# Performance work log

Measured on AMD Instinct MI355X. Metric: run time of the kernel, lower is better.

The kernel has to match this reference:

```python
import jax, jax.numpy as jnp
import numpy as np


def setup_inputs() -> dict:
    key = jax.random.key(0)
    k1, k2 = jax.random.split(key)
    B, N, C = 16, 2049, 1024
    x = jax.random.normal(k1, (B, N, C), dtype=jnp.float32)
    # nn.Linear(dim, 3*dim, bias=False): weight applied as x @ W^T; store as (C, 3C)
    w_qkv = jax.random.normal(k2, (C, 3 * C), dtype=jnp.float32) * (1.0 / np.sqrt(C))
    return {"x": x, "w_qkv": w_qkv}


def reference(x, w_qkv):
    B, N, C = x.shape
    scale = C ** (-0.5)
    qkv = (x @ w_qkv).reshape(B, N, 3, C)  # [B,N,3,C]
    q = qkv[:, :, 0, :]  # [B,N,C]
    k = qkv[:, :, 1, :]  # [B,N,C]
    # Original computes full q @ k^T then keeps only row 0, cols 1: before softmax.
    # Mathematically identical (and efficient) to use only the CLS query row.
    q_cls = q[:, 0, :]                                   # [B,C]
    attn_cls_logits = jnp.einsum('bc,bnc->bn', q_cls, k[:, 1:, :]) * scale  # [B,N-1]
    return jax.nn.softmax(attn_cls_logits, axis=-1)
```

## Files before the change

### kernel.cpp

```cpp
#include <hip/hip_runtime.h>
#include <math.h>


#define BATCH 16
#define SEQ   2049
#define CH    1024
#define W3    3072
#define NOUT  2048


__global__ __launch_bounds__(64) void qcls_partial_kernel(
    const float* __restrict__ x, const float* __restrict__ w,
    float* __restrict__ part) {
    const int ci = blockIdx.x;
    const int pi = blockIdx.y;
    const int lane = threadIdx.x;
    const int d0 = pi * 16;
    __shared__ float xs[BATCH * 16];
    #pragma unroll
    for (int i = lane; i < BATCH * 16; i += 64) {
        const int b = i >> 4, dd = i & 15;
        xs[i] = x[(size_t)b * SEQ * CH + d0 + dd];
    }
    __syncthreads();
    const int c = ci * 256 + lane * 4;
    float4 acc[BATCH];
    #pragma unroll
    for (int b = 0; b < BATCH; ++b) acc[b] = {0.f, 0.f, 0.f, 0.f};
    #pragma unroll 4
    for (int dd = 0; dd < 16; ++dd) {
        const float4 wv = *(const float4*)(w + (size_t)(d0 + dd) * W3 + c);
        #pragma unroll
        for (int b = 0; b < BATCH; ++b) {
            const float s = xs[b * 16 + dd];
            acc[b].x += s * wv.x; acc[b].y += s * wv.y;
            acc[b].z += s * wv.z; acc[b].w += s * wv.w;
        }
    }
    #pragma unroll
    for (int b = 0; b < BATCH; ++b)
        *(float4*)(part + (size_t)pi * BATCH * CH + b * CH + c) = acc[b];
}

__global__ __launch_bounds__(256) void qcls_reduce_kernel(
    const float* __restrict__ part, float* __restrict__ qcls) {
    const int id = blockIdx.x * 256 + threadIdx.x;
    float s = 0.f;
    #pragma unroll 8
    for (int p = 0; p < 64; ++p) s += part[(size_t)p * BATCH * CH + id];
    qcls[id] = s;
}

__global__ __launch_bounds__(256) void v_kernel(
    const float* __restrict__ w, const float* __restrict__ qcls,
    float* __restrict__ v) {
    __shared__ float qs[BATCH * CH];
    const int t = threadIdx.x;
    for (int i = t; i < BATCH * CH; i += 256) qs[i] = qcls[i];
    __syncthreads();
    const int lane = t & 63;
    const int wave = t >> 6;
    #pragma unroll
    for (int k = 0; k < 2; ++k) {
        const int d = blockIdx.x * 8 + wave * 2 + k;
        const float* wrow = w + (size_t)d * W3 + CH;
        float4 wv[4];
        #pragma unroll
        for (int j = 0; j < 4; ++j)
            wv[j] = *(const float4*)(wrow + lane * 4 + j * 256);
        #pragma unroll
        for (int b = 0; b < BATCH; ++b) {
            float acc = 0.f;
            #pragma unroll
            for (int j = 0; j < 4; ++j) {
                float4 qv = *(const float4*)(&qs[b * CH + lane * 4 + j * 256]);
                acc += wv[j].x * qv.x + wv[j].y * qv.y
                     + wv[j].z * qv.z + wv[j].w * qv.w;
            }
            #pragma unroll
            for (int off = 32; off > 0; off >>= 1)
                acc += __shfl_down(acc, off, 64);
            if (lane == 0) v[b * CH + d] = acc;
        }
    }
}

__global__ __launch_bounds__(256) void logits_kernel(
    const float* __restrict__ x, const float* __restrict__ v,
    float* __restrict__ logits) {
    const int t = threadIdx.x;
    const int lane = t & 63;
    const int row = blockIdx.x * 4 + (t >> 6);
    const int b = row >> 11;
    const int n = row & 2047;
    const float* xrow = x + ((size_t)b * SEQ + n + 1) * CH;
    const float* vrow = v + b * CH;
    float acc = 0.f;
    #pragma unroll
    for (int j = 0; j < 4; ++j) {
        float4 xv = *(const float4*)(xrow + lane * 4 + j * 256);
        float4 vv = *(const float4*)(vrow + lane * 4 + j * 256);
        acc += xv.x * vv.x + xv.y * vv.y + xv.z * vv.z + xv.w * vv.w;
    }
    #pragma unroll
    for (int off = 32; off > 0; off >>= 1)
        acc += __shfl_down(acc, off, 64);
    if (lane == 0) logits[row] = acc * 0.03125f;
}

__global__ __launch_bounds__(256) void softmax_kernel(
    const float* __restrict__ logits, float* __restrict__ out) {
    const int b = blockIdx.x;
    const int t = threadIdx.x;
    __shared__ float sm[256];
    float val[8];
    float m = -1e30f;
    #pragma unroll
    for (int i = 0; i < 8; ++i) {
        val[i] = logits[b * NOUT + t + i * 256];
        m = fmaxf(m, val[i]);
    }
    sm[t] = m; __syncthreads();
    for (int s = 128; s > 0; s >>= 1) {
        if (t < s) sm[t] = fmaxf(sm[t], sm[t + s]);
        __syncthreads();
    }
    const float mx = sm[0];
    __syncthreads();
    float e[8];
    float sum = 0.f;
    #pragma unroll
    for (int i = 0; i < 8; ++i) { e[i] = expf(val[i] - mx); sum += e[i]; }
    sm[t] = sum; __syncthreads();
    for (int s = 128; s > 0; s >>= 1) {
        if (t < s) sm[t] += sm[t + s];
        __syncthreads();
    }
    const float inv = 1.0f / sm[0];
    #pragma unroll
    for (int i = 0; i < 8; ++i) out[b * NOUT + t + i * 256] = e[i] * inv;
}

extern "C" void kernel_launch(void* const* d_in, const int* in_sizes, int n_in,
                              void* d_out, int out_size, void* d_ws, size_t ws_size,
                              hipStream_t stream) {
    const float* x = (const float*)d_in[0];
    const float* w = (const float*)d_in[1];
    float* out = (float*)d_out;
    float* ws = (float*)d_ws;

    float* part   = ws;
    float* qcls   = ws + 1048576;
    float* vbuf   = ws + 1048576 + 16384;
    float* logits = ws + 1048576 + 32768;

    qcls_partial_kernel<<<dim3(4, 64), 64, 0, stream>>>(x, w, part);
    qcls_reduce_kernel<<<64, 256, 0, stream>>>(part, qcls);
    v_kernel<<<128, 256, 0, stream>>>(w, qcls, vbuf);
    logits_kernel<<<8192, 256, 0, stream>>>(x, vbuf, logits);
    softmax_kernel<<<BATCH, 256, 0, stream>>>(logits, out);
}
```

Baseline: 219.4 us.

## Reduce q_cls partials in-block and fold final reduction into v kernel

The q_cls partial kernel now uses 512-thread blocks that split the D dimension across 8 waves and reduce across waves in shared memory, cutting partial slices from 64 to 8. The separate reduce kernel is dropped; v_kernel sums the 8 partials while loading q into shared memory and handles 16 rows per block over 64 blocks. logits_kernel stages the per-batch v vector in shared memory. The aim is to remove one launch and the partial-buffer traffic, at the cost of fewer blocks (32) in the first stage and 64 blocks redundantly reducing the partials.

```diff
diff --git a/kernel.cpp b/kernel.cpp
--- a/kernel.cpp
+++ b/kernel.cpp
@@ -7,75 +7,100 @@
 #define CH    1024
 #define W3    3072
 #define NOUT  2048
+#define PD    8
 
 
-__global__ __launch_bounds__(64) void qcls_partial_kernel(
+__global__ __launch_bounds__(512) void qcls_part_kernel(
     const float* __restrict__ x, const float* __restrict__ w,
     float* __restrict__ part) {
     const int ci = blockIdx.x;
     const int pi = blockIdx.y;
-    const int lane = threadIdx.x;
-    const int d0 = pi * 16;
-    __shared__ float xs[BATCH * 16];
-    #pragma unroll
-    for (int i = lane; i < BATCH * 16; i += 64) {
-        const int b = i >> 4, dd = i & 15;
-        xs[i] = x[(size_t)b * SEQ * CH + d0 + dd];
+    const int t  = threadIdx.x;
+    const int lane = t & 63;
+    const int wv   = t >> 6;
+
+    __shared__ float  xs[BATCH][128];
+    __shared__ float4 red[8][8][64];
+
+    for (int i = t; i < BATCH * 128; i += 512) {
+        const int b = i >> 7, dd = i & 127;
+        xs[b][dd] = x[(size_t)b * SEQ * CH + pi * 128 + dd];
     }
     __syncthreads();
+
     const int c = ci * 256 + lane * 4;
     float4 acc[BATCH];
     #pragma unroll
     for (int b = 0; b < BATCH; ++b) acc[b] = {0.f, 0.f, 0.f, 0.f};
+
+    const int drow0 = pi * 128 + wv * 16;
     #pragma unroll 4
     for (int dd = 0; dd < 16; ++dd) {
-        const float4 wv = *(const float4*)(w + (size_t)(d0 + dd) * W3 + c);
+        const float4 wvec = *(const float4*)(w + (size_t)(drow0 + dd) * W3 + c);
+        const int dl = wv * 16 + dd;
         #pragma unroll
         for (int b = 0; b < BATCH; ++b) {
-            const float s = xs[b * 16 + dd];
-            acc[b].x += s * wv.x; acc[b].y += s * wv.y;
-            acc[b].z += s * wv.z; acc[b].w += s * wv.w;
+            const float s = xs[b][dl];
+            acc[b].x += s * wvec.x; acc[b].y += s * wvec.y;
+            acc[b].z += s * wvec.z; acc[b].w += s * wvec.w;
         }
     }
+
     #pragma unroll
-    for (int b = 0; b < BATCH; ++b)
-        *(float4*)(part + (size_t)pi * BATCH * CH + b * CH + c) = acc[b];
-}
-
-__global__ __launch_bounds__(256) void qcls_reduce_kernel(
-    const float* __restrict__ part, float* __restrict__ qcls) {
-    const int id = blockIdx.x * 256 + threadIdx.x;
-    float s = 0.f;
-    #pragma unroll 8
-    for (int p = 0; p < 64; ++p) s += part[(size_t)p * BATCH * CH + id];
-    qcls[id] = s;
+    for (int p = 0; p < 2; ++p) {
+        #pragma unroll
+        for (int b2 = 0; b2 < 8; ++b2)
+            red[wv][b2][lane] = acc[p * 8 + b2];
+        __syncthreads();
+        {
+            const int b = p * 8 + wv;
+            float4 s = red[0][wv][lane];
+            #pragma unroll
+            for (int ww = 1; ww < 8; ++ww) {
+                const float4 r = red[ww][wv][lane];
+                s.x += r.x; s.y += r.y; s.z += r.z; s.w += r.w;
+            }
+            *(float4*)(part + ((size_t)pi * BATCH + b) * CH + c) = s;
+        }
+        __syncthreads();
+    }
 }
 
 __global__ __launch_bounds__(256) void v_kernel(
-    const float* __restrict__ w, const float* __restrict__ qcls,
+    const float* __restrict__ w, const float* __restrict__ part,
     float* __restrict__ v) {
     __shared__ float qs[BATCH * CH];
     const int t = threadIdx.x;
-    for (int i = t; i < BATCH * CH; i += 256) qs[i] = qcls[i];
+    const float4* p4 = (const float4*)part;
+    for (int i4 = t; i4 < BATCH * CH / 4; i4 += 256) {
+        float4 s = p4[i4];
+        #pragma unroll
+        for (int p = 1; p < PD; ++p) {
+            const float4 r = p4[p * (BATCH * CH / 4) + i4];
+            s.x += r.x; s.y += r.y; s.z += r.z; s.w += r.w;
+        }
+        ((float4*)qs)[i4] = s;
+    }
     __syncthreads();
+
     const int lane = t & 63;
     const int wave = t >> 6;
     #pragma unroll
-    for (int k = 0; k < 2; ++k) {
-        const int d = blockIdx.x * 8 + wave * 2 + k;
+    for (int k = 0; k < 4; ++k) {
+        const int d = blockIdx.x * 16 + wave * 4 + k;
         const float* wrow = w + (size_t)d * W3 + CH;
-        float4 wv[4];
+        float4 wv4[4];
         #pragma unroll
         for (int j = 0; j < 4; ++j)
-            wv[j] = *(const float4*)(wrow + lane * 4 + j * 256);
+            wv4[j] = *(const float4*)(wrow + lane * 4 + j * 256);
         #pragma unroll
         for (int b = 0; b < BATCH; ++b) {
             float acc = 0.f;
             #pragma unroll
             for (int j = 0; j < 4; ++j) {
-                float4 qv = *(const float4*)(&qs[b * CH + lane * 4 + j * 256]);
-                acc += wv[j].x * qv.x + wv[j].y * qv.y
-                     + wv[j].z * qv.z + wv[j].w * qv.w;
+                const float4 qv = *(const float4*)(&qs[b * CH + lane * 4 + j * 256]);
+                acc += wv4[j].x * qv.x + wv4[j].y * qv.y
+                     + wv4[j].z * qv.z + wv4[j].w * qv.w;
             }
             #pragma unroll
             for (int off = 32; off > 0; off >>= 1)
@@ -90,16 +115,21 @@
     float* __restrict__ logits) {
     const int t = threadIdx.x;
     const int lane = t & 63;
-    const int row = blockIdx.x * 4 + (t >> 6);
-    const int b = row >> 11;
-    const int n = row & 2047;
+    const int row0 = blockIdx.x * 4;
+    const int b = row0 >> 11;
+
+    __shared__ float4 vs[CH / 4];
+    vs[t] = ((const float4*)(v + (size_t)b * CH))[t];
+    __syncthreads();
+
+    const int row = row0 + (t >> 6);
+    const int n = row & (NOUT - 1);
     const float* xrow = x + ((size_t)b * SEQ + n + 1) * CH;
-    const float* vrow = v + b * CH;
     float acc = 0.f;
     #pragma unroll
     for (int j = 0; j < 4; ++j) {
-        float4 xv = *(const float4*)(xrow + lane * 4 + j * 256);
-        float4 vv = *(const float4*)(vrow + lane * 4 + j * 256);
+        const float4 xv = *(const float4*)(xrow + lane * 4 + j * 256);
+        const float4 vv = vs[lane + j * 64];
         acc += xv.x * vv.x + xv.y * vv.y + xv.z * vv.z + xv.w * vv.w;
     }
     #pragma unroll
@@ -150,13 +180,11 @@
     float* ws = (float*)d_ws;
 
     float* part   = ws;
-    float* qcls   = ws + 1048576;
-    float* vbuf   = ws + 1048576 + 16384;
-    float* logits = ws + 1048576 + 32768;
+    float* vbuf   = ws + 131072;
+    float* logits = ws + 147456;
 
-    qcls_partial_kernel<<<dim3(4, 64), 64, 0, stream>>>(x, w, part);
-    qcls_reduce_kernel<<<64, 256, 0, stream>>>(part, qcls);
-    v_kernel<<<128, 256, 0, stream>>>(w, qcls, vbuf);
+    qcls_part_kernel<<<dim3(4, 8), 512, 0, stream>>>(x, w, part);
+    v_kernel<<<64, 256, 0, stream>>>(w, part, vbuf);
     logits_kernel<<<8192, 256, 0, stream>>>(x, vbuf, logits);
     softmax_kernel<<<BATCH, 256, 0, stream>>>(logits, out);
 }
```

Result: slower. 230.4 us (+5.0%).
